# Kernel tuning notes

Hardware: AMD Instinct MI355X
Metric: run time of the kernel (lower is better)

## Reference

```python
import jax, jax.numpy as jnp
import numpy as np

N_EDGE_CLOSEST = 4

def setup_inputs() -> dict:
    key = jax.random.key(0)
    ks = jax.random.split(key, 8)
    B, N_SEND, N_REC, K, D, E_EMB, LIN_OUT = 2, 49152, 115200, N_EDGE_CLOSEST, 256, 64, 256
    E = N_REC * K
    LIN_IN = D + E_EMB  # 320
    x = jax.random.normal(ks[0], (B, N_SEND, D), dtype=jnp.float32)
    # buffers produced by get_decoder_edge_details: edge_attr = arange(E) % K, knn edge index
    edge_attr = (jnp.arange(E, dtype=jnp.float32) % K).reshape(E, 1)
    edge_src = jax.random.randint(ks[1], (E,), 0, N_SEND, dtype=jnp.int32)
    edge_dst = jnp.repeat(jnp.arange(N_REC, dtype=jnp.int32), K)  # each receiver has K incoming edges
    s = lambda fi, fo: 1.0 / np.sqrt(fi)
    w1e = jax.random.normal(ks[2], (1, E_EMB), dtype=jnp.float32) * s(1, E_EMB)
    b1e = jnp.zeros((E_EMB,), dtype=jnp.float32)
    w2e = jax.random.normal(ks[3], (E_EMB, E_EMB), dtype=jnp.float32) * s(E_EMB, E_EMB)
    b2e = jnp.zeros((E_EMB,), dtype=jnp.float32)
    w1f = jax.random.normal(ks[4], (LIN_IN, LIN_OUT), dtype=jnp.float32) * s(LIN_IN, LIN_OUT)
    b1f = jnp.zeros((LIN_OUT,), dtype=jnp.float32)
    w2f = jax.random.normal(ks[5], (LIN_OUT, LIN_OUT), dtype=jnp.float32) * s(LIN_OUT, LIN_OUT)
    b2f = jnp.zeros((LIN_OUT,), dtype=jnp.float32)
    return {"x": x, "edge_attr": edge_attr, "w1e": w1e, "b1e": b1e, "w2e": w2e, "b2e": b2e,
            "w1f": w1f, "b1f": b1f, "w2f": w2f, "b2f": b2f,
            "edge_src": edge_src, "edge_dst": edge_dst}


def reference(x, edge_attr, w1e, b1e, w2e, b2e, w1f, b1f, w2f, b2f, edge_src, edge_dst):
    E = edge_dst.shape[0]
    n_rec = E // N_EDGE_CLOSEST  # static: knn gives exactly K edges per receiver
    # edge embedder MLP: Linear -> SiLU -> Linear, on [E, 1]
    edge_feat = jax.nn.silu(edge_attr @ w1e + b1e) @ w2e + b2e          # [E, E_EMB]
    v_s = x[:, edge_src, :]                                              # gather: [B, E, D]
    edge_feat_b = jnp.broadcast_to(edge_feat[None], (x.shape[0],) + edge_feat.shape)
    v_s_prime = jnp.concatenate([v_s, edge_feat_b], axis=-1)             # [B, E, D+E_EMB]
    # scatter_sum over receivers (axis 1)
    seg = lambda v: jax.ops.segment_sum(v, edge_dst, num_segments=n_rec)
    v_m_sum = jax.vmap(seg)(v_s_prime)                                   # [B, n_rec, D+E_EMB]
    # FeedForward: Linear -> SiLU -> Linear
    out = jax.nn.silu(v_m_sum @ w1f + b1f) @ w2f + b2f                   # [B, n_rec, LIN_OUT]
    return out
```

## Files before the change

### kernel.cpp

```cpp
#include <hip/hip_runtime.h>

#define NSND   49152
#define NRECV  115200
#define NSROWS (2 * NSND)
#define NRROWS (2 * NRECV)

typedef __bf16 bx8 __attribute__((ext_vector_type(8)));
typedef float  fx4 __attribute__((ext_vector_type(4)));

__device__ __forceinline__ unsigned short f2bf(float f) {
  unsigned u = __float_as_uint(f);
  u += 0x7FFFu + ((u >> 16) & 1u);
  return (unsigned short)(u >> 16);
}

__global__ void prep_c1(const float* __restrict__ w1e, const float* __restrict__ b1e,
                        const float* __restrict__ w2e, const float* __restrict__ b2e,
                        const float* __restrict__ w1f, const float* __restrict__ b1f,
                        float* __restrict__ c1) {
  __shared__ float s_sum[64];
  __shared__ float s_ef[64];
  int t = threadIdx.x;
  if (t < 64) {
    float w = w1e[t], b = b1e[t];
    float acc = 0.f;
    for (int k = 0; k < 4; ++k) {
      float v = (float)k * w + b;
      acc += v / (1.f + expf(-v));
    }
    s_sum[t] = acc;
  }
  __syncthreads();
  if (t < 64) {
    float acc = 4.f * b2e[t];
    for (int j = 0; j < 64; ++j) acc += s_sum[j] * w2e[j * 64 + t];
    s_ef[t] = acc;
  }
  __syncthreads();
  if (t < 256) {
    float acc = b1f[t];
    for (int i = 0; i < 64; ++i) acc += s_ef[i] * w1f[(256 + i) * 256 + t];
    c1[t] = acc;
  }
}

__global__ void prep_w(const float* __restrict__ w1f, const float* __restrict__ w2f,
                       unsigned short* __restrict__ W1f, unsigned short* __restrict__ W2f) {
  int idx  = blockIdx.x * blockDim.x + threadIdx.x;
  int lane = idx & 63;
  int ks   = (idx >> 6) & 7;
  int ct   = idx >> 9;
  int n     = ct * 16 + (lane & 15);
  int kbase = ks * 32 + (lane >> 4) * 8;
  unsigned p1[4], p2[4];
#pragma unroll
  for (int h = 0; h < 4; ++h) {
    int k = kbase + 2 * h;
    p1[h] = (unsigned)f2bf(w1f[k * 256 + n]) | ((unsigned)f2bf(w1f[(k + 1) * 256 + n]) << 16);
    p2[h] = (unsigned)f2bf(w2f[k * 256 + n]) | ((unsigned)f2bf(w2f[(k + 1) * 256 + n]) << 16);
  }
  *(uint4*)(W1f + (size_t)idx * 8) = make_uint4(p1[0], p1[1], p1[2], p1[3]);
  *(uint4*)(W2f + (size_t)idx * 8) = make_uint4(p2[0], p2[1], p2[2], p2[3]);
}

__global__ __launch_bounds__(512, 2) void k1_senders(
    const float* __restrict__ x, const float* __restrict__ c1,
    const unsigned short* __restrict__ W1f, unsigned short* __restrict__ Yp) {
  __shared__ char lds[65536];

  const int lane = threadIdx.x & 63;
  const int wv   = threadIdx.x >> 6;
  const int row  = lane & 15;
  const int kg   = lane >> 4;
  const int rb   = blockIdx.x * 128;

  const float* xr = x + (size_t)(rb + wv * 16 + row) * 256;
  bx8 hfr[8];
#pragma unroll
  for (int ks = 0; ks < 8; ++ks) {
    fx4 a = __builtin_nontemporal_load((const fx4*)(xr + ks * 32 + kg * 8));
    fx4 c = __builtin_nontemporal_load((const fx4*)(xr + ks * 32 + kg * 8 + 4));
    unsigned p0 = (unsigned)f2bf(a.x) | ((unsigned)f2bf(a.y) << 16);
    unsigned p1 = (unsigned)f2bf(a.z) | ((unsigned)f2bf(a.w) << 16);
    unsigned p2 = (unsigned)f2bf(c.x) | ((unsigned)f2bf(c.y) << 16);
    unsigned p3 = (unsigned)f2bf(c.z) | ((unsigned)f2bf(c.w) << 16);
    uint4 pu = make_uint4(p0, p1, p2, p3);
    hfr[ks] = *(bx8*)&pu;
  }

  fx4 acc[16];
#pragma unroll
  for (int nc = 0; nc < 16; ++nc) acc[nc] = (fx4){0.f, 0.f, 0.f, 0.f};

#pragma unroll
  for (int i = 0; i < 8; ++i) {
    unsigned off = (unsigned)(wv * 8192 + i * 1024 + lane * 16);
    *(uint4*)(lds + off) = *(const uint4*)((const char*)W1f + off);
  }
  __syncthreads();
#pragma unroll
  for (int ks = 0; ks < 8; ++ks) {
#pragma unroll
    for (int q = 0; q < 8; ++q) {
      bx8 wfr = *(const bx8*)(lds + (unsigned)((q * 8 + ks) * 1024 + lane * 16));
      acc[q] = __builtin_amdgcn_mfma_f32_16x16x32_bf16(wfr, hfr[ks], acc[q], 0, 0, 0);
    }
  }
  __syncthreads();

#pragma unroll
  for (int i = 0; i < 8; ++i) {
    unsigned off = (unsigned)(wv * 8192 + i * 1024 + lane * 16);
    *(uint4*)(lds + off) = *(const uint4*)((const char*)W1f + 65536 + off);
  }
  __syncthreads();
#pragma unroll
  for (int ks = 0; ks < 8; ++ks) {
#pragma unroll
    for (int q = 0; q < 8; ++q) {
      bx8 wfr = *(const bx8*)(lds + (unsigned)((q * 8 + ks) * 1024 + lane * 16));
      acc[8 + q] = __builtin_amdgcn_mfma_f32_16x16x32_bf16(wfr, hfr[ks], acc[8 + q], 0, 0, 0);
    }
  }
  __syncthreads();

  const fx4* c1_4 = (const fx4*)c1;
#pragma unroll
  for (int nc = 0; nc < 16; ++nc) {
    fx4 cv = c1_4[nc * 4 + kg];
    unsigned lo = (unsigned)f2bf(acc[nc][0] + 0.25f * cv.x)
                | ((unsigned)f2bf(acc[nc][1] + 0.25f * cv.y) << 16);
    unsigned hi = (unsigned)f2bf(acc[nc][2] + 0.25f * cv.z)
                | ((unsigned)f2bf(acc[nc][3] + 0.25f * cv.w) << 16);
    unsigned sb = (unsigned)(wv * 8192 + row * 512 + nc * 32 + kg * 8)
                ^ (unsigned)((row & 7) << 4);
    *(uint2*)(lds + sb) = make_uint2(lo, hi);
  }
#pragma unroll
  for (int i = 0; i < 8; ++i) {
    int srow  = 2 * i + (lane >> 5);
    int chunk = lane & 31;
    unsigned sb = (unsigned)(wv * 8192 + srow * 512 + chunk * 16)
                ^ (unsigned)((srow & 7) << 4);
    uint4 v = *(const uint4*)(lds + sb);
    *(uint4*)(Yp + (size_t)(rb + wv * 16 + srow) * 256 + chunk * 8) = v;
  }
}

__global__ __launch_bounds__(512, 2) void k23_recv(
    const unsigned short* __restrict__ Yp, const int* __restrict__ edge_src,
    const unsigned short* __restrict__ W2f, const float* __restrict__ b2f,
    float* __restrict__ out) {
  __shared__ char lds[65536];

  const int tid  = threadIdx.x;
  const int lane = tid & 63;
  const int wv   = tid >> 6;
  const int row  = lane & 15;
  const int kg   = lane >> 4;

  const int blk = blockIdx.x;
  const int b   = blk / 900;
  const int rr0 = (blk % 900) * 128;
  const unsigned short* yb = Yp + (size_t)b * NSND * 256;

  int4 s = ((const int4*)edge_src)[rr0 + wv * 16 + row];
  const unsigned short* y0 = yb + (size_t)s.x * 256 + kg * 8;
  const unsigned short* y1 = yb + (size_t)s.y * 256 + kg * 8;
  const unsigned short* y2 = yb + (size_t)s.z * 256 + kg * 8;
  const unsigned short* y3 = yb + (size_t)s.w * 256 + kg * 8;

  bx8 hfr[8];
#pragma unroll
  for (int g = 0; g < 2; ++g) {
    bx8 d[4][4];
#pragma unroll
    for (int t = 0; t < 4; ++t) {
      int ks = g * 4 + t;
      d[t][0] = *(const bx8*)(y0 + ks * 32);
      d[t][1] = *(const bx8*)(y1 + ks * 32);
      d[t][2] = *(const bx8*)(y2 + ks * 32);
      d[t][3] = *(const bx8*)(y3 + ks * 32);
    }
    __builtin_amdgcn_sched_barrier(0);
#pragma unroll
    for (int t = 0; t < 4; ++t) {
      int ks = g * 4 + t;
      unsigned p[4];
#pragma unroll
      for (int h = 0; h < 4; ++h) {
        float v0 = (float)d[t][0][2*h] + (float)d[t][1][2*h] + (float)d[t][2][2*h] + (float)d[t][3][2*h];
        float v1 = (float)d[t][0][2*h+1] + (float)d[t][1][2*h+1] + (float)d[t][2][2*h+1] + (float)d[t][3][2*h+1];
        float h0 = v0 / (1.f + __expf(-v0));
        float h1 = v1 / (1.f + __expf(-v1));
        p[h] = (unsigned)f2bf(h0) | ((unsigned)f2bf(h1) << 16);
      }
      uint4 pu = make_uint4(p[0], p[1], p[2], p[3]);
      hfr[ks] = *(bx8*)&pu;
    }
  }

#pragma unroll
  for (int i = 0; i < 8; ++i) {
    unsigned off = (unsigned)(wv * 8192 + i * 1024 + lane * 16);
    uint4 v = *(const uint4*)((const char*)W2f + off);
    *(uint4*)(lds + off) = v;
  }
  __syncthreads();

  fx4 acc[16];
#pragma unroll
  for (int nc = 0; nc < 16; ++nc) acc[nc] = (fx4){0.f, 0.f, 0.f, 0.f};

#pragma unroll
  for (int ks = 0; ks < 8; ++ks) {
#pragma unroll
    for (int q = 0; q < 8; ++q) {
      bx8 wfr = *(const bx8*)(lds + (unsigned)((q * 8 + ks) * 1024 + lane * 16));
      acc[q] = __builtin_amdgcn_mfma_f32_16x16x32_bf16(wfr, hfr[ks], acc[q], 0, 0, 0);
    }
  }
  __syncthreads();

#pragma unroll
  for (int i = 0; i < 8; ++i) {
    unsigned off = (unsigned)(wv * 8192 + i * 1024 + lane * 16);
    uint4 v = *(const uint4*)((const char*)W2f + 65536 + off);
    *(uint4*)(lds + off) = v;
  }
  __syncthreads();

#pragma unroll
  for (int ks = 0; ks < 8; ++ks) {
#pragma unroll
    for (int q = 0; q < 8; ++q) {
      bx8 wfr = *(const bx8*)(lds + (unsigned)((q * 8 + ks) * 1024 + lane * 16));
      acc[8 + q] = __builtin_amdgcn_mfma_f32_16x16x32_bf16(wfr, hfr[ks], acc[8 + q], 0, 0, 0);
    }
  }
  __syncthreads();

  const fx4* b2f4 = (const fx4*)b2f;
  const size_t orow0 = ((size_t)b * NRECV + rr0 + wv * 16) * 256;
#pragma unroll
  for (int p = 0; p < 2; ++p) {
#pragma unroll
    for (int q = 0; q < 8; ++q) {
      int nc = p * 8 + q;
      fx4 o = acc[nc] + b2f4[nc * 4 + kg];
      unsigned sb = (unsigned)(wv * 8192 + row * 512 + q * 64 + kg * 16)
                  ^ (unsigned)((row & 7) << 4);
      *(fx4*)(lds + sb) = o;
    }
#pragma unroll
    for (int i = 0; i < 8; ++i) {
      int srow  = 2 * i + (lane >> 5);
      int chunk = lane & 31;
      unsigned sb = (unsigned)(wv * 8192 + srow * 512 + chunk * 16)
                  ^ (unsigned)((srow & 7) << 4);
      fx4 v = *(const fx4*)(lds + sb);
      __builtin_nontemporal_store(v, (fx4*)(out + orow0 + (size_t)srow * 256 + p * 128 + chunk * 4));
    }
  }
}

__global__ __launch_bounds__(256, 4) void heal_fused(
    const float* __restrict__ x, const int* __restrict__ edge_src,
    const float* __restrict__ c1, const unsigned short* __restrict__ W1f,
    const unsigned short* __restrict__ W2f, const float* __restrict__ b2f,
    float* __restrict__ out) {
  __shared__ char lds[64 * 512];
  const int lane = threadIdx.x & 63;
  const int wv   = threadIdx.x >> 6;
  const int blk = blockIdx.x;
  const int b   = blk / 1800;
  const int r0  = (blk % 1800) * 64;
  const float* xb = x + (size_t)b * NSND * 256;
#pragma unroll 4
  for (int i = 0; i < 16; ++i) {
    int row = wv * 16 + i;
    int r   = r0 + row;
    int4 s  = *(const int4*)(edge_src + 4 * (size_t)r);
    float4 a0 = *((const float4*)(xb + (size_t)s.x * 256) + lane);
    float4 a1 = *((const float4*)(xb + (size_t)s.y * 256) + lane);
    float4 a2 = *((const float4*)(xb + (size_t)s.z * 256) + lane);
    float4 a3 = *((const float4*)(xb + (size_t)s.w * 256) + lane);
    float v0 = a0.x + a1.x + a2.x + a3.x;
    float v1 = a0.y + a1.y + a2.y + a3.y;
    float v2 = a0.z + a1.z + a2.z + a3.z;
    float v3 = a0.w + a1.w + a2.w + a3.w;
    unsigned lo = (unsigned)f2bf(v0) | ((unsigned)f2bf(v1) << 16);
    unsigned hi = (unsigned)f2bf(v2) | ((unsigned)f2bf(v3) << 16);
    unsigned byte = (unsigned)(row * 512 + lane * 8) ^ (unsigned)((row & 7) << 4);
    *(uint2*)(lds + byte) = make_uint2(lo, hi);
  }
  fx4 acc[16];
#pragma unroll
  for (int nc = 0; nc < 16; ++nc) acc[nc] = (fx4){0.f, 0.f, 0.f, 0.f};
  const bx8* W1v = (const bx8*)W1f;
  const int arow = wv * 16 + (lane & 15);
  const unsigned aswz = (unsigned)((arow & 7) << 4);
  const unsigned alin = (unsigned)(arow * 512 + (lane >> 4) * 16);
#pragma unroll
  for (int ks = 0; ks < 8; ++ks) {
    bx8 afr = *(const bx8*)(lds + ((alin + ks * 64) ^ aswz));
#pragma unroll
    for (int nc = 0; nc < 16; ++nc) {
      bx8 bfr = W1v[(nc * 8 + ks) * 64 + lane];
      acc[nc] = __builtin_amdgcn_mfma_f32_16x16x32_bf16(afr, bfr, acc[nc], 0, 0, 0);
    }
  }
  float c1v[16];
#pragma unroll
  for (int nc = 0; nc < 16; ++nc) c1v[nc] = c1[nc * 16 + (lane & 15)];
#pragma unroll
  for (int nc = 0; nc < 16; ++nc) {
    int hcol = nc * 16 + (lane & 15);
#pragma unroll
    for (int j = 0; j < 4; ++j) {
      float v = acc[nc][j] + c1v[nc];
      float h = v / (1.f + __expf(-v));
      int hrow = wv * 16 + (lane >> 4) * 4 + j;
      unsigned hb = (unsigned)(hrow * 512 + hcol * 2) ^ (unsigned)((hrow & 7) << 4);
      *(unsigned short*)(lds + hb) = f2bf(h);
    }
  }
#pragma unroll
  for (int nc = 0; nc < 16; ++nc) acc[nc] = (fx4){0.f, 0.f, 0.f, 0.f};
  const bx8* W2v = (const bx8*)W2f;
#pragma unroll
  for (int ks = 0; ks < 8; ++ks) {
    bx8 afr = *(const bx8*)(lds + ((alin + ks * 64) ^ aswz));
#pragma unroll
    for (int nc = 0; nc < 16; ++nc) {
      bx8 bfr = W2v[(nc * 8 + ks) * 64 + lane];
      acc[nc] = __builtin_amdgcn_mfma_f32_16x16x32_bf16(afr, bfr, acc[nc], 0, 0, 0);
    }
  }
  size_t obase = ((size_t)b * NRECV + r0) * 256;
#pragma unroll
  for (int nc = 0; nc < 16; ++nc) {
    int col = nc * 16 + (lane & 15);
    float bias = b2f[col];
#pragma unroll
    for (int j = 0; j < 4; ++j) {
      int row = wv * 16 + (lane >> 4) * 4 + j;
      out[obase + (size_t)row * 256 + col] = acc[nc][j] + bias;
    }
  }
}

extern "C" void kernel_launch(void* const* d_in, const int* in_sizes, int n_in,
                              void* d_out, int out_size, void* d_ws, size_t ws_size,
                              hipStream_t stream) {
  const float* x    = (const float*)d_in[0];
  const float* w1e  = (const float*)d_in[2];
  const float* b1e  = (const float*)d_in[3];
  const float* w2e  = (const float*)d_in[4];
  const float* b2e  = (const float*)d_in[5];
  const float* w1f  = (const float*)d_in[6];
  const float* b1f  = (const float*)d_in[7];
  const float* w2f  = (const float*)d_in[8];
  const float* b2f  = (const float*)d_in[9];
  const int* edge_src = (const int*)d_in[10];
  float* out = (float*)d_out;

  char* ws = (char*)d_ws;
  float* c1            = (float*)ws;
  unsigned short* W1f  = (unsigned short*)(ws + 4096);
  unsigned short* W2f  = (unsigned short*)(ws + 4096 + 131072);
  unsigned short* Yp   = (unsigned short*)(ws + 1048576);
  const size_t need = 1048576 + (size_t)NSROWS * 256 * 2;

  hipLaunchKernelGGL(prep_c1, dim3(1), dim3(256), 0, stream, w1e, b1e, w2e, b2e, w1f, b1f, c1);
  hipLaunchKernelGGL(prep_w, dim3(32), dim3(256), 0, stream, w1f, w2f, W1f, W2f);
  if (ws_size >= need) {
    hipLaunchKernelGGL(k1_senders, dim3(NSROWS / 128), dim3(512), 0, stream, x, c1, W1f, Yp);
    hipLaunchKernelGGL(k23_recv, dim3(NRROWS / 128), dim3(512), 0, stream,
                       Yp, edge_src, W2f, b2f, out);
  } else {
    hipLaunchKernelGGL(heal_fused, dim3(NRROWS / 64), dim3(256), 0, stream,
                       x, edge_src, c1, W1f, W2f, b2f, out);
  }
}
```

Before: 163.3 us.

## Split receiver stage into separate gather+SiLU and dense GEMM kernels

Replaces the fused receiver kernel with two kernels. The first gathers and sums four sender rows per receiver, applies SiLU and writes a bf16 intermediate H to workspace. The second runs the 256x256 second linear layer with MFMA over H. This is meant to separate the latency-bound gather from the MFMA work so each kernel gets its own occupancy and scheduling, at the cost of an extra write and read of a roughly 118 MB intermediate and one more launch. It is only taken when the workspace is large enough.

```diff
diff --git a/kernel.cpp b/kernel.cpp
--- a/kernel.cpp
+++ b/kernel.cpp
@@ -144,6 +144,125 @@
                 ^ (unsigned)((srow & 7) << 4);
     uint4 v = *(const uint4*)(lds + sb);
     *(uint4*)(Yp + (size_t)(rb + wv * 16 + srow) * 256 + chunk * 8) = v;
+  }
+}
+
+__global__ __launch_bounds__(256, 4) void kA_gather(
+    const unsigned short* __restrict__ Yp, const int* __restrict__ edge_src,
+    unsigned short* __restrict__ H) {
+  const int tid0 = blockIdx.x * 256 + threadIdx.x;
+  const int4* esrc4 = (const int4*)edge_src;
+
+#pragma unroll
+  for (int it = 0; it < 3; ++it) {
+    bx8 d[4][4];
+    int rows[4], chunks[4];
+#pragma unroll
+    for (int j = 0; j < 4; ++j) {
+      int task  = tid0 + (it * 4 + j) * 614400;
+      int row   = task >> 5;
+      int chunk = task & 31;
+      rows[j] = row; chunks[j] = chunk;
+      int bb = row >= NRECV;
+      int rr = row - bb * NRECV;
+      int4 s = esrc4[rr];
+      const unsigned short* yb = Yp + (size_t)bb * NSND * 256;
+      d[j][0] = *(const bx8*)(yb + (size_t)s.x * 256 + chunk * 8);
+      d[j][1] = *(const bx8*)(yb + (size_t)s.y * 256 + chunk * 8);
+      d[j][2] = *(const bx8*)(yb + (size_t)s.z * 256 + chunk * 8);
+      d[j][3] = *(const bx8*)(yb + (size_t)s.w * 256 + chunk * 8);
+    }
+    __builtin_amdgcn_sched_barrier(0);
+#pragma unroll
+    for (int j = 0; j < 4; ++j) {
+      unsigned p[4];
+#pragma unroll
+      for (int h = 0; h < 4; ++h) {
+        float v0 = (float)d[j][0][2*h] + (float)d[j][1][2*h] + (float)d[j][2][2*h] + (float)d[j][3][2*h];
+        float v1 = (float)d[j][0][2*h+1] + (float)d[j][1][2*h+1] + (float)d[j][2][2*h+1] + (float)d[j][3][2*h+1];
+        float h0 = v0 / (1.f + __expf(-v0));
+        float h1 = v1 / (1.f + __expf(-v1));
+        p[h] = (unsigned)f2bf(h0) | ((unsigned)f2bf(h1) << 16);
+      }
+      *(uint4*)(H + (size_t)rows[j] * 256 + chunks[j] * 8) = make_uint4(p[0], p[1], p[2], p[3]);
+    }
+  }
+}
+
+__global__ __launch_bounds__(512, 2) void kB_dense(
+    const unsigned short* __restrict__ H, const unsigned short* __restrict__ W2f,
+    const float* __restrict__ b2f, float* __restrict__ out) {
+  __shared__ char lds[65536];
+
+  const int lane = threadIdx.x & 63;
+  const int wv   = threadIdx.x >> 6;
+  const int row  = lane & 15;
+  const int kg   = lane >> 4;
+  const int rb   = blockIdx.x * 128;
+
+  const unsigned short* hr = H + (size_t)(rb + wv * 16 + row) * 256;
+  bx8 hfr[8];
+#pragma unroll
+  for (int ks = 0; ks < 8; ++ks)
+    hfr[ks] = *(const bx8*)(hr + ks * 32 + kg * 8);
+
+  fx4 acc[16];
+#pragma unroll
+  for (int nc = 0; nc < 16; ++nc) acc[nc] = (fx4){0.f, 0.f, 0.f, 0.f};
+
+#pragma unroll
+  for (int i = 0; i < 8; ++i) {
+    unsigned off = (unsigned)(wv * 8192 + i * 1024 + lane * 16);
+    *(uint4*)(lds + off) = *(const uint4*)((const char*)W2f + off);
+  }
+  __syncthreads();
+#pragma unroll
+  for (int ks = 0; ks < 8; ++ks) {
+#pragma unroll
+    for (int q = 0; q < 8; ++q) {
+      bx8 wfr = *(const bx8*)(lds + (unsigned)((q * 8 + ks) * 1024 + lane * 16));
+      acc[q] = __builtin_amdgcn_mfma_f32_16x16x32_bf16(wfr, hfr[ks], acc[q], 0, 0, 0);
+    }
+  }
+  __syncthreads();
+
+#pragma unroll
+  for (int i = 0; i < 8; ++i) {
+    unsigned off = (unsigned)(wv * 8192 + i * 1024 + lane * 16);
+    *(uint4*)(lds + off) = *(const uint4*)((const char*)W2f + 65536 + off);
+  }
+  __syncthreads();
+#pragma unroll
+  for (int ks = 0; ks < 8; ++ks) {
+#pragma unroll
+    for (int q = 0; q < 8; ++q) {
+      bx8 wfr = *(const bx8*)(lds + (unsigned)((q * 8 + ks) * 1024 + lane * 16));
+      acc[8 + q] = __builtin_amdgcn_mfma_f32_16x16x32_bf16(wfr, hfr[ks], acc[8 + q], 0, 0, 0);
+    }
+  }
+  __syncthreads();
+
+  const fx4* b2f4 = (const fx4*)b2f;
+  const size_t orow0 = (size_t)(rb + wv * 16) * 256;
+#pragma unroll
+  for (int p = 0; p < 2; ++p) {
+#pragma unroll
+    for (int q = 0; q < 8; ++q) {
+      int nc = p * 8 + q;
+      fx4 o = acc[nc] + b2f4[nc * 4 + kg];
+      unsigned sb = (unsigned)(wv * 8192 + row * 512 + q * 64 + kg * 16)
+                  ^ (unsigned)((row & 7) << 4);
+      *(fx4*)(lds + sb) = o;
+    }
+#pragma unroll
+    for (int i = 0; i < 8; ++i) {
+      int srow  = 2 * i + (lane >> 5);
+      int chunk = lane & 31;
+      unsigned sb = (unsigned)(wv * 8192 + srow * 512 + chunk * 16)
+                  ^ (unsigned)((srow & 7) << 4);
+      fx4 v = *(const fx4*)(lds + sb);
+      __builtin_nontemporal_store(v, (fx4*)(out + orow0 + (size_t)srow * 256 + p * 128 + chunk * 4));
+    }
   }
 }
 
@@ -370,11 +489,17 @@
   unsigned short* W1f  = (unsigned short*)(ws + 4096);
   unsigned short* W2f  = (unsigned short*)(ws + 4096 + 131072);
   unsigned short* Yp   = (unsigned short*)(ws + 1048576);
-  const size_t need = 1048576 + (size_t)NSROWS * 256 * 2;
+  unsigned short* H    = (unsigned short*)(ws + 1048576 + (size_t)NSROWS * 256 * 2);
+  const size_t need_old = 1048576 + (size_t)NSROWS * 256 * 2;
+  const size_t need_big = need_old + (size_t)NRROWS * 256 * 2;
 
   hipLaunchKernelGGL(prep_c1, dim3(1), dim3(256), 0, stream, w1e, b1e, w2e, b2e, w1f, b1f, c1);
   hipLaunchKernelGGL(prep_w, dim3(32), dim3(256), 0, stream, w1f, w2f, W1f, W2f);
-  if (ws_size >= need) {
+  if (ws_size >= need_big) {
+    hipLaunchKernelGGL(k1_senders, dim3(NSROWS / 128), dim3(512), 0, stream, x, c1, W1f, Yp);
+    hipLaunchKernelGGL(kA_gather, dim3(2400), dim3(256), 0, stream, Yp, edge_src, H);
+    hipLaunchKernelGGL(kB_dense, dim3(NRROWS / 128), dim3(512), 0, stream, H, W2f, b2f, out);
+  } else if (ws_size >= need_old) {
     hipLaunchKernelGGL(k1_senders, dim3(NSROWS / 128), dim3(512), 0, stream, x, c1, W1f, Yp);
     hipLaunchKernelGGL(k23_recv, dim3(NRROWS / 128), dim3(512), 0, stream,
                        Yp, edge_src, W2f, b2f, out);
```

New measurement: 219.0 us. +34.1%, slower.
